# Kernel optimization log

Hardware: AMD Instinct MI355X
Metric: run time of the kernel (lower is better)

The kernel has to match this reference:

```python
import jax, jax.numpy as jnp
import numpy as np

GAMMA = 0.9865


def setup_inputs() -> dict:
    key = jax.random.key(0)
    ks = jax.random.split(key, 6)
    B, T, DIN, D = 8, 2048, 1024, 1024
    return {
        "xq": jax.random.normal(ks[0], (B, T, DIN), dtype=jnp.float32),
        "xk": jax.random.normal(ks[1], (B, T, DIN), dtype=jnp.float32),
        "xv": jax.random.normal(ks[2], (B, T, DIN), dtype=jnp.float32),
        "Wq": jax.random.normal(ks[3], (DIN, D), dtype=jnp.float32) * (DIN ** -0.5),
        "Wk": jax.random.normal(ks[4], (DIN, D), dtype=jnp.float32) * (DIN ** -0.5),
        "Wv": jax.random.normal(ks[5], (DIN, D), dtype=jnp.float32) * (DIN ** -0.5),
    }


def reference(xq, xk, xv, Wq, Wk, Wv):
    # Dense projections (no bias)
    Q = jnp.einsum("btd,de->bte", xq, Wq)  # [B,T,D]
    K = jnp.einsum("btd,de->bte", xk, Wk)
    V = jnp.einsum("btd,de->bte", xv, Wv)

    # einsum('ib,bj->bj', K_t^T, V_t) == (sum_i K[b,t,i]) * V[b,t,:]
    ksum = jnp.sum(K, axis=-1)            # [B,T]
    u = ksum[..., None] * V               # [B,T,D]
    # recurrence starts at t=1 with s[0]=0, so u[0] never contributes
    u = u * (jnp.arange(u.shape[1]) > 0)[None, :, None]

    def step(s, u_t):
        s = s * jnp.float32(GAMMA) + u_t
        return s, s

    s0 = jnp.zeros(u.shape[::2], dtype=u.dtype)          # [B,D]
    _, S = jax.lax.scan(step, s0, jnp.swapaxes(u, 0, 1))  # S: [T,B,D]
    return Q * jnp.swapaxes(S, 0, 1)                      # [B,T,D]
```

## Files before the change

kernel.cpp:

```cpp
#include <hip/hip_runtime.h>
#include <hip/hip_bf16.h>

#define GAMMA 0.9865f

typedef __attribute__((ext_vector_type(8))) short bf16x8;
typedef __attribute__((ext_vector_type(4))) float f32x4;

static constexpr int Bb  = 8;
static constexpr int Tt  = 2048;
static constexpr int DIN = 1024;
static constexpr int Dd  = 1024;
static constexpr int Mm  = Bb * Tt;
static constexpr int CL  = 64;
static constexpr int NC  = Tt / CL;
static constexpr int NT  = DIN / 64;

__device__ __forceinline__ void gload16(const void* g, void* l) {
  __builtin_amdgcn_global_load_lds(
      (const __attribute__((address_space(1))) void*)g,
      (__attribute__((address_space(3))) void*)l, 16, 0, 0);
}

__device__ __forceinline__ void bar() {
  asm volatile("" ::: "memory");
  __builtin_amdgcn_s_barrier();
  asm volatile("" ::: "memory");
}

__global__ __launch_bounds__(256) void prep_kernel(
    const float* __restrict__ Wq, const float* __restrict__ Wk,
    const float* __restrict__ Wv, float* __restrict__ wsum,
    __hip_bfloat16* __restrict__ Wt) {
  int bid = blockIdx.x;
  if (bid < 256) {
    int row  = bid * 4 + (threadIdx.x >> 6);
    int lane = threadIdx.x & 63;
    const float4* rp = (const float4*)(Wk + (size_t)row * DIN);
    float s = 0.f;
#pragma unroll
    for (int i = 0; i < 4; ++i) {
      float4 v = rp[lane + i * 64];
      s += v.x + v.y + v.z + v.w;
    }
    for (int off = 32; off; off >>= 1) s += __shfl_down(s, off);
    if (lane == 0) wsum[row] = s;
    return;
  }
  int wid = bid - 256;
  int z = wid >> 10, rem = wid & 1023;
  int kb = rem & 31, nb = rem >> 5;
  const float* W = z ? Wv : Wq;
  __hip_bfloat16* outp = Wt + (size_t)z * DIN * Dd;
  __shared__ float tile[32][33];
  int k0 = kb * 32, n0 = nb * 32;
  int tx = threadIdx.x & 31, ty = threadIdx.x >> 5;
#pragma unroll
  for (int i = 0; i < 4; ++i)
    tile[ty + i * 8][tx] = W[(size_t)(k0 + ty + i * 8) * Dd + n0 + tx];
  __syncthreads();
#pragma unroll
  for (int i = 0; i < 4; ++i)
    outp[(size_t)(n0 + ty + i * 8) * DIN + k0 + tx] =
        __float2bfloat16(tile[tx][ty + i * 8]);
}

__global__ __launch_bounds__(256) void castksum_kernel(
    const float* __restrict__ xq, const float* __restrict__ xk,
    const float* __restrict__ xv, const float* __restrict__ wsum,
    __hip_bfloat16* __restrict__ oq, __hip_bfloat16* __restrict__ ov,
    float* __restrict__ ksum) {
  int y = blockIdx.y;
  if (y < 2) {
    const float* src = y ? xv : xq;
    __hip_bfloat16* dst = y ? ov : oq;
    size_t i = (size_t)blockIdx.x * 256 + threadIdx.x;
    const float4* p = (const float4*)src;
    float4 a = p[i * 2], b = p[i * 2 + 1];
    union { __hip_bfloat16 h[8]; bf16x8 v; } u;
    u.h[0] = __float2bfloat16(a.x); u.h[1] = __float2bfloat16(a.y);
    u.h[2] = __float2bfloat16(a.z); u.h[3] = __float2bfloat16(a.w);
    u.h[4] = __float2bfloat16(b.x); u.h[5] = __float2bfloat16(b.y);
    u.h[6] = __float2bfloat16(b.z); u.h[7] = __float2bfloat16(b.w);
    ((bf16x8*)dst)[i] = u.v;
    return;
  }
  if (blockIdx.x >= Mm / 4) return;
  int row  = blockIdx.x * 4 + (threadIdx.x >> 6);
  int lane = threadIdx.x & 63;
  const float4* rp = (const float4*)(xk + (size_t)row * DIN);
  const float4* wp = (const float4*)wsum;
  float s = 0.f;
#pragma unroll
  for (int i = 0; i < 4; ++i) {
    float4 a = rp[lane + i * 64];
    float4 w = wp[lane + i * 64];
    s += a.x * w.x + a.y * w.y + a.z * w.z + a.w * w.w;
  }
  for (int off = 32; off; off >>= 1) s += __shfl_down(s, off);
  if (lane == 0) ksum[row] = s;
}

__device__ __forceinline__ void stage_half(const __hip_bfloat16* g, char* l, int tid) {
#pragma unroll
  for (int j = 0; j < 2; ++j) {
    int c = tid + j * 512;
    int row = c >> 3, ch = c & 7;
    gload16(g + (size_t)row * DIN + ((ch ^ (row & 7)) << 3), l + c * 16);
  }
}

__device__ __forceinline__ bf16x8 lds_frag(const char* base, int row, int kc) {
  return *(const bf16x8*)(base + (((row << 3) + (kc ^ (row & 7))) << 4));
}

#define MFMA_QUAD(MLO, NLO)                                                  \
  _Pragma("unroll") for (int mi = 0; mi < 4; ++mi)                           \
  _Pragma("unroll") for (int ni = 0; ni < 2; ++ni)                           \
  _Pragma("unroll") for (int ks = 0; ks < 2; ++ks)                           \
      acc[(MLO) + mi][(NLO) + ni] = __builtin_amdgcn_mfma_f32_16x16x32_bf16( \
          a[(MLO) + mi][ks], b[(NLO) + ni][ks], acc[(MLO) + mi][(NLO) + ni], 0, 0, 0);

__global__ __launch_bounds__(512, 2) void gemm8_kernel(
    const __hip_bfloat16* __restrict__ Aq, const __hip_bfloat16* __restrict__ Av,
    const __hip_bfloat16* __restrict__ Wt,
    __hip_bfloat16* __restrict__ Qbf, __hip_bfloat16* __restrict__ Vbf) {
  extern __shared__ char lds[];

  int lin = blockIdx.x;
  int wg  = (lin & 7) * 64 + (lin >> 3);
  int z   = wg >> 8, rem = wg & 255;
  int by  = rem & 3, bx = rem >> 2;

  const __hip_bfloat16* Ab = z ? Av : Aq;
  const int m0 = bx * 256, n0 = by * 256;
  const __hip_bfloat16* Ag = Ab + (size_t)m0 * DIN;
  const __hip_bfloat16* Bg = Wt + ((size_t)z * Dd + n0) * DIN;
  __hip_bfloat16* Cc = z ? Vbf : Qbf;

  const int tid = threadIdx.x;
  const int wv = tid >> 6, lane = tid & 63;
  const int wm = (wv >> 2) * 128, wn = (wv & 3) * 64;
  const int fq = lane >> 4, fr = lane & 15;

  f32x4 acc[8][4] = {};

  stage_half(Ag,                  lds,                 tid);
  stage_half(Ag + 128 * DIN,      lds + 16384,         tid);
  stage_half(Bg,                  lds + 32768,         tid);
  stage_half(Bg + 128 * DIN,      lds + 49152,         tid);
  stage_half(Ag + 64,             lds + 65536,         tid);
  stage_half(Ag + 128 * DIN + 64, lds + 65536 + 16384, tid);
  asm volatile("s_waitcnt vmcnt(4)" ::: "memory");
  bar();

  for (int t = 0; t < NT; ++t) {
    char* buf  = lds + (t & 1) * 65536;
    char* bufN = lds + ((t + 1) & 1) * 65536;
    const char* At = buf;
    const char* Bt = buf + 32768;
    bf16x8 a[8][2], b[4][2];

#pragma unroll
    for (int mi = 0; mi < 4; ++mi)
#pragma unroll
      for (int ks = 0; ks < 2; ++ks)
        a[mi][ks] = lds_frag(At, wm + mi * 16 + fr, ks * 4 + fq);
#pragma unroll
    for (int ni = 0; ni < 2; ++ni)
#pragma unroll
      for (int ks = 0; ks < 2; ++ks)
        b[ni][ks] = lds_frag(Bt, wn + ni * 16 + fr, ks * 4 + fq);
    if (t + 1 < NT) stage_half(Bg + (size_t)(t + 1) * 64, bufN + 32768, tid);
    bar();
    __builtin_amdgcn_s_setprio(1);
    MFMA_QUAD(0, 0);
    __builtin_amdgcn_s_setprio(0);
    bar();

#pragma unroll
    for (int mi = 4; mi < 8; ++mi)
#pragma unroll
      for (int ks = 0; ks < 2; ++ks)
        a[mi][ks] = lds_frag(At, wm + mi * 16 + fr, ks * 4 + fq);
    if (t + 1 < NT)
      stage_half(Bg + 128 * DIN + (size_t)(t + 1) * 64, bufN + 49152, tid);
    bar();
    __builtin_amdgcn_s_setprio(1);
    MFMA_QUAD(4, 0);
    __builtin_amdgcn_s_setprio(0);
    bar();

#pragma unroll
    for (int ni = 2; ni < 4; ++ni)
#pragma unroll
      for (int ks = 0; ks < 2; ++ks)
        b[ni][ks] = lds_frag(Bt, wn + ni * 16 + fr, ks * 4 + fq);
    if (t + 2 < NT) stage_half(Ag + (size_t)(t + 2) * 64, buf, tid);
    bar();
    __builtin_amdgcn_s_setprio(1);
    MFMA_QUAD(0, 2);
    __builtin_amdgcn_s_setprio(0);
    bar();

    if (t + 2 < NT)
      stage_half(Ag + 128 * DIN + (size_t)(t + 2) * 64, buf + 16384, tid);
    if (t + 1 < NT) {
      if (t + 2 < NT) asm volatile("s_waitcnt vmcnt(4)" ::: "memory");
      else            asm volatile("s_waitcnt vmcnt(0)" ::: "memory");
    }
    bar();
    __builtin_amdgcn_s_setprio(1);
    MFMA_QUAD(4, 2);
    __builtin_amdgcn_s_setprio(0);
    bar();
  }

#pragma unroll
  for (int mi = 0; mi < 8; ++mi) {
#pragma unroll
    for (int ni = 0; ni < 4; ++ni) {
      f32x4 v = acc[mi][ni];
      int row = m0 + wm + mi * 16 + fq * 4;
      int col = n0 + wn + ni * 16 + fr;
#pragma unroll
      for (int j = 0; j < 4; ++j)
        Cc[(size_t)(row + j) * Dd + col] = __float2bfloat16(v[j]);
    }
  }
}

__global__ void scanA_kernel(const __hip_bfloat16* __restrict__ Vbf,
                             const float* __restrict__ ksum,
                             float* __restrict__ E) {
  int b = blockIdx.x, c = blockIdx.y;
  int d = blockIdx.z * 256 + threadIdx.x;
  const __hip_bfloat16* Vp = Vbf + ((size_t)(b * Tt + c * CL) * Dd) + d;
  const float* kp = ksum + b * Tt + c * CL;
  float s = 0.f;
#pragma unroll 8
  for (int t = 0; t < CL; ++t) {
    float u = kp[t] * __bfloat162float(Vp[(size_t)t * Dd]);
    if (c == 0 && t == 0) u = 0.f;
    s = s * GAMMA + u;
  }
  E[((size_t)b * NC + c) * Dd + d] = s;
}

__global__ void scanB_kernel(const float* __restrict__ E, float* __restrict__ carry,
                             float gCL) {
  int b = blockIdx.x;
  int d = blockIdx.y * 256 + threadIdx.x;
  float send = 0.f;
  for (int c = 0; c < NC; ++c) {
    size_t idx = ((size_t)b * NC + c) * Dd + d;
    float e = E[idx];
    carry[idx] = send;
    send = e + gCL * send;
  }
}

__global__ void final_kernel(const __hip_bfloat16* __restrict__ Vbf,
                             const __hip_bfloat16* __restrict__ Qbf,
                             const float* __restrict__ ksum,
                             const float* __restrict__ carry,
                             float* __restrict__ outp) {
  int b = blockIdx.x, c = blockIdx.y;
  int d = blockIdx.z * 256 + threadIdx.x;
  size_t base = ((size_t)(b * Tt + c * CL) * Dd) + d;
  float s = carry[((size_t)b * NC + c) * Dd + d];
  const float* kp = ksum + b * Tt + c * CL;
#pragma unroll 4
  for (int t = 0; t < CL; ++t) {
    float u = kp[t] * __bfloat162float(Vbf[base + (size_t)t * Dd]);
    if (c == 0 && t == 0) u = 0.f;
    s = s * GAMMA + u;
    outp[base + (size_t)t * Dd] = __bfloat162float(Qbf[base + (size_t)t * Dd]) * s;
  }
}

extern "C" void kernel_launch(void* const* d_in, const int* in_sizes, int n_in,
                              void* d_out, int out_size, void* d_ws, size_t ws_size,
                              hipStream_t stream) {
  (void)in_sizes; (void)n_in; (void)out_size; (void)ws_size;
  const float* xq = (const float*)d_in[0];
  const float* xk = (const float*)d_in[1];
  const float* xv = (const float*)d_in[2];
  const float* Wq = (const float*)d_in[3];
  const float* Wk = (const float*)d_in[4];
  const float* Wv = (const float*)d_in[5];
  float* outp = (float*)d_out;

  char* ws = (char*)d_ws;
  size_t off = 0;
  auto alloc = [&](size_t bytes) {
    char* p = ws + off;
    off += (bytes + 255) & ~(size_t)255;
    return p;
  };
  __hip_bfloat16* xq_bf = (__hip_bfloat16*)alloc((size_t)Mm * DIN * 2);
  __hip_bfloat16* xv_bf = (__hip_bfloat16*)alloc((size_t)Mm * DIN * 2);
  __hip_bfloat16* Wt    = (__hip_bfloat16*)alloc((size_t)2 * DIN * Dd * 2);
  __hip_bfloat16* Qbf   = (__hip_bfloat16*)alloc((size_t)Mm * Dd * 2);
  __hip_bfloat16* Vbf   = (__hip_bfloat16*)alloc((size_t)Mm * Dd * 2);
  float* wsum  = (float*)alloc((size_t)DIN * 4);
  float* ksum  = (float*)alloc((size_t)Mm * 4);
  float* E     = (float*)alloc((size_t)Bb * NC * Dd * 4);
  float* carry = (float*)alloc((size_t)Bb * NC * Dd * 4);

  double g = 1.0;
  for (int i = 0; i < CL; ++i) g *= (double)GAMMA;
  float gCL = (float)g;

  (void)hipFuncSetAttribute((const void*)gemm8_kernel,
                            hipFuncAttributeMaxDynamicSharedMemorySize, 131072);

  prep_kernel<<<256 + 2048, 256, 0, stream>>>(Wq, Wk, Wv, wsum, Wt);
  castksum_kernel<<<dim3(Mm * DIN / 8 / 256, 3), 256, 0, stream>>>(
      xq, xk, xv, wsum, xq_bf, xv_bf, ksum);
  gemm8_kernel<<<512, 512, 131072, stream>>>(xq_bf, xv_bf, Wt, Qbf, Vbf);
  scanA_kernel<<<dim3(Bb, NC, Dd / 256), 256, 0, stream>>>(Vbf, ksum, E);
  scanB_kernel<<<dim3(Bb, Dd / 256), 256, 0, stream>>>(E, carry, gCL);
  final_kernel<<<dim3(Bb, NC, Dd / 256), 256, 0, stream>>>(Vbf, Qbf, ksum, carry, outp);
}
```

Before: 151.5 us.

## Fuse chunk-local scan and output multiply into Q projection GEMM epilogue

New measurement: 147.3 us. 1.03x faster.

```diff
diff --git a/kernel.cpp b/kernel.cpp
--- a/kernel.cpp
+++ b/kernel.cpp
@@ -25,6 +25,10 @@
   asm volatile("" ::: "memory");
   __builtin_amdgcn_s_barrier();
   asm volatile("" ::: "memory");
+}
+
+__device__ __forceinline__ float bf16_to_f32(unsigned short u) {
+  return __uint_as_float(((unsigned int)u) << 16);
 }
 
 __global__ __launch_bounds__(256) void prep_kernel(
@@ -120,30 +124,10 @@
       acc[(MLO) + mi][(NLO) + ni] = __builtin_amdgcn_mfma_f32_16x16x32_bf16( \
           a[(MLO) + mi][ks], b[(NLO) + ni][ks], acc[(MLO) + mi][(NLO) + ni], 0, 0, 0);
 
-__global__ __launch_bounds__(512, 2) void gemm8_kernel(
-    const __hip_bfloat16* __restrict__ Aq, const __hip_bfloat16* __restrict__ Av,
-    const __hip_bfloat16* __restrict__ Wt,
-    __hip_bfloat16* __restrict__ Qbf, __hip_bfloat16* __restrict__ Vbf) {
-  extern __shared__ char lds[];
-
-  int lin = blockIdx.x;
-  int wg  = (lin & 7) * 64 + (lin >> 3);
-  int z   = wg >> 8, rem = wg & 255;
-  int by  = rem & 3, bx = rem >> 2;
-
-  const __hip_bfloat16* Ab = z ? Av : Aq;
-  const int m0 = bx * 256, n0 = by * 256;
-  const __hip_bfloat16* Ag = Ab + (size_t)m0 * DIN;
-  const __hip_bfloat16* Bg = Wt + ((size_t)z * Dd + n0) * DIN;
-  __hip_bfloat16* Cc = z ? Vbf : Qbf;
-
-  const int tid = threadIdx.x;
-  const int wv = tid >> 6, lane = tid & 63;
-  const int wm = (wv >> 2) * 128, wn = (wv & 3) * 64;
-  const int fq = lane >> 4, fr = lane & 15;
-
-  f32x4 acc[8][4] = {};
-
+__device__ __forceinline__ void gemm_core(const __hip_bfloat16* Ag,
+                                          const __hip_bfloat16* Bg, char* lds,
+                                          int tid, int wm, int wn, int fq, int fr,
+                                          f32x4 (&acc)[8][4]) {
   stage_half(Ag,                  lds,                 tid);
   stage_half(Ag + 128 * DIN,      lds + 16384,         tid);
   stage_half(Bg,                  lds + 32768,         tid);
@@ -214,6 +198,26 @@
     __builtin_amdgcn_s_setprio(0);
     bar();
   }
+}
+
+__global__ __launch_bounds__(512, 2) void gemmV_kernel(
+    const __hip_bfloat16* __restrict__ Av, const __hip_bfloat16* __restrict__ Wt,
+    __hip_bfloat16* __restrict__ Vbf) {
+  extern __shared__ char lds[];
+  int lin = blockIdx.x;
+  int wg  = (lin & 7) * 32 + (lin >> 3);
+  int by  = wg & 3, bx = wg >> 2;
+  const int m0 = bx * 256, n0 = by * 256;
+  const __hip_bfloat16* Ag = Av + (size_t)m0 * DIN;
+  const __hip_bfloat16* Bg = Wt + ((size_t)Dd + n0) * DIN;
+
+  const int tid = threadIdx.x;
+  const int wv = tid >> 6, lane = tid & 63;
+  const int wm = (wv >> 2) * 128, wn = (wv & 3) * 64;
+  const int fq = lane >> 4, fr = lane & 15;
+
+  f32x4 acc[8][4] = {};
+  gemm_core(Ag, Bg, lds, tid, wm, wn, fq, fr, acc);
 
 #pragma unroll
   for (int mi = 0; mi < 8; ++mi) {
@@ -224,7 +228,75 @@
       int col = n0 + wn + ni * 16 + fr;
 #pragma unroll
       for (int j = 0; j < 4; ++j)
-        Cc[(size_t)(row + j) * Dd + col] = __float2bfloat16(v[j]);
+        Vbf[(size_t)(row + j) * Dd + col] = __float2bfloat16(v[j]);
+    }
+  }
+}
+
+__global__ __launch_bounds__(512, 2) void gemmQ_kernel(
+    const __hip_bfloat16* __restrict__ Aq, const __hip_bfloat16* __restrict__ Wt,
+    const __hip_bfloat16* __restrict__ Vbf, const float* __restrict__ ksum,
+    const float* __restrict__ carry, float* __restrict__ outp) {
+  extern __shared__ char lds[];
+  int lin = blockIdx.x;
+  int wg  = (lin & 7) * 32 + (lin >> 3);
+  int by  = wg & 3, bx = wg >> 2;
+  const int m0 = bx * 256, n0 = by * 256;
+  const __hip_bfloat16* Ag = Aq + (size_t)m0 * DIN;
+  const __hip_bfloat16* Bg = Wt + (size_t)n0 * DIN;
+
+  const int tid = threadIdx.x;
+  const int wv = tid >> 6, lane = tid & 63;
+  const int wm = (wv >> 2) * 128, wn = (wv & 3) * 64;
+  const int fq = lane >> 4, fr = lane & 15;
+
+  f32x4 acc[8][4] = {};
+  gemm_core(Ag, Bg, lds, tid, wm, wn, fq, fr, acc);
+
+  const int b = m0 >> 11, t0 = m0 & 2047;
+#pragma unroll
+  for (int j = 0; j < 16; ++j) {
+    int c = tid + j * 512;
+    int row = c >> 5, s = c & 31;
+    int chn = s ^ (row & 7);
+    gload16(Vbf + (size_t)(m0 + row) * Dd + n0 + chn * 8, lds + c * 16);
+  }
+  asm volatile("s_waitcnt vmcnt(0)" ::: "memory");
+  bar();
+
+#pragma unroll
+  for (int p = 0; p < 2; ++p) {
+    int task = tid + p * 512;
+    int col = task & 255, cc = task >> 8;
+    float s = carry[((size_t)b * NC + (t0 >> 6) + cc) * Dd + n0 + col];
+    const float* kp = ksum + (size_t)b * Tt + t0 + cc * 64;
+    for (int i = 0; i < CL; ++i) {
+      int t = cc * 64 + i;
+      int addr = t * 512 + ((col * 2) ^ ((t & 7) << 4));
+      unsigned short* sp = (unsigned short*)(lds + addr);
+      float v = bf16_to_f32(*sp);
+      float kv = kp[i];
+      if (t0 == 0 && cc == 0 && i == 0) kv = 0.f;
+      s = s * GAMMA + kv * v;
+      *sp = (unsigned short)(__bfloat16_as_ushort(__float2bfloat16(s)));
+    }
+  }
+  bar();
+
+#pragma unroll
+  for (int mi = 0; mi < 8; ++mi) {
+#pragma unroll
+    for (int ni = 0; ni < 4; ++ni) {
+      f32x4 v = acc[mi][ni];
+      int row = wm + mi * 16 + fq * 4;
+      int col = wn + ni * 16 + fr;
+#pragma unroll
+      for (int j = 0; j < 4; ++j) {
+        int r = row + j;
+        int addr = r * 512 + ((col * 2) ^ ((r & 7) << 4));
+        float S = bf16_to_f32(*(const unsigned short*)(lds + addr));
+        outp[(size_t)(m0 + r) * Dd + n0 + col] = v[j] * S;
+      }
     }
   }
 }
@@ -259,25 +331,6 @@
   }
 }
 
-__global__ void final_kernel(const __hip_bfloat16* __restrict__ Vbf,
-                             const __hip_bfloat16* __restrict__ Qbf,
-                             const float* __restrict__ ksum,
-                             const float* __restrict__ carry,
-                             float* __restrict__ outp) {
-  int b = blockIdx.x, c = blockIdx.y;
-  int d = blockIdx.z * 256 + threadIdx.x;
-  size_t base = ((size_t)(b * Tt + c * CL) * Dd) + d;
-  float s = carry[((size_t)b * NC + c) * Dd + d];
-  const float* kp = ksum + b * Tt + c * CL;
-#pragma unroll 4
-  for (int t = 0; t < CL; ++t) {
-    float u = kp[t] * __bfloat162float(Vbf[base + (size_t)t * Dd]);
-    if (c == 0 && t == 0) u = 0.f;
-    s = s * GAMMA + u;
-    outp[base + (size_t)t * Dd] = __bfloat162float(Qbf[base + (size_t)t * Dd]) * s;
-  }
-}
-
 extern "C" void kernel_launch(void* const* d_in, const int* in_sizes, int n_in,
                               void* d_out, int out_size, void* d_ws, size_t ws_size,
                               hipStream_t stream) {
@@ -300,7 +353,6 @@
   __hip_bfloat16* xq_bf = (__hip_bfloat16*)alloc((size_t)Mm * DIN * 2);
   __hip_bfloat16* xv_bf = (__hip_bfloat16*)alloc((size_t)Mm * DIN * 2);
   __hip_bfloat16* Wt    = (__hip_bfloat16*)alloc((size_t)2 * DIN * Dd * 2);
-  __hip_bfloat16* Qbf   = (__hip_bfloat16*)alloc((size_t)Mm * Dd * 2);
   __hip_bfloat16* Vbf   = (__hip_bfloat16*)alloc((size_t)Mm * Dd * 2);
   float* wsum  = (float*)alloc((size_t)DIN * 4);
   float* ksum  = (float*)alloc((size_t)Mm * 4);
@@ -311,14 +363,16 @@
   for (int i = 0; i < CL; ++i) g *= (double)GAMMA;
   float gCL = (float)g;
 
-  (void)hipFuncSetAttribute((const void*)gemm8_kernel,
+  (void)hipFuncSetAttribute((const void*)gemmV_kernel,
+                            hipFuncAttributeMaxDynamicSharedMemorySize, 131072);
+  (void)hipFuncSetAttribute((const void*)gemmQ_kernel,
                             hipFuncAttributeMaxDynamicSharedMemorySize, 131072);
 
   prep_kernel<<<256 + 2048, 256, 0, stream>>>(Wq, Wk, Wv, wsum, Wt);
   castksum_kernel<<<dim3(Mm * DIN / 8 / 256, 3), 256, 0, stream>>>(
       xq, xk, xv, wsum, xq_bf, xv_bf, ksum);
-  gemm8_kernel<<<512, 512, 131072, stream>>>(xq_bf, xv_bf, Wt, Qbf, Vbf);
+  gemmV_kernel<<<256, 512, 131072, stream>>>(xv_bf, Wt, Vbf);
   scanA_kernel<<<dim3(Bb, NC, Dd / 256), 256, 0, stream>>>(Vbf, ksum, E);
   scanB_kernel<<<dim3(Bb, Dd / 256), 256, 0, stream>>>(E, carry, gCL);
-  final_kernel<<<dim3(Bb, NC, Dd / 256), 256, 0, stream>>>(Vbf, Qbf, ksum, carry, outp);
-}
+  gemmQ_kernel<<<256, 512, 131072, stream>>>(xq_bf, Wt, Vbf, ksum, carry, outp);
+}
```
